# Kernel optimization log

Measured on AMD Instinct MI355X. Metric: run time of the kernel, lower is better.

The kernel has to match this reference:

```python
import jax, jax.numpy as jnp
import numpy as np

B, S, D, H = 2, 2048, 1024, 16
DEPTH = D // H


def setup_inputs() -> dict:
    key = jax.random.key(0)
    ks = jax.random.split(key, 6)
    q = jax.random.normal(ks[0], (B, S, D), dtype=jnp.float32)
    k = jax.random.normal(ks[1], (B, S, D), dtype=jnp.float32)
    v = jax.random.normal(ks[2], (B, S, D), dtype=jnp.float32)
    # causal mask, broadcastable to [B, H, S, S]
    mask = jnp.tril(jnp.ones((S, S), dtype=bool))[None, None, :, :]
    wq = jax.random.normal(ks[3], (D, D), dtype=jnp.float32)
    wk = jax.random.normal(ks[4], (D, D), dtype=jnp.float32)
    wv = jax.random.normal(ks[5], (D, D), dtype=jnp.float32)
    return {"q": q, "k": k, "v": v, "mask": mask, "wq": wq, "wk": wk, "wv": wv}


def _split_heads(x):
    # [B, S, D] -> [B, H, S, depth]
    return x.reshape(x.shape[0], -1, H, DEPTH).transpose(0, 2, 1, 3)


def reference(q, k, v, mask, wq, wk, wv):
    q = _split_heads(q @ wq)
    k = _split_heads(k @ wk)
    v = _split_heads(v @ wv)
    scale = jnp.sqrt(jnp.float32(DEPTH))
    # [B, H, S, S]
    scores = jnp.einsum("bhqd,bhkd->bhqk", q, k) / scale
    scores = jnp.where(mask, scores, jnp.float32(-8.0))
    scores = scores - jnp.max(scores, axis=-1, keepdims=True)
    attn = jax.nn.softmax(scores, axis=-1)
    out = jnp.einsum("bhqk,bhkd->bhqd", attn, v)
    # [B, H, S, depth] -> [B, S, D]
    return out.transpose(0, 2, 1, 3).reshape(out.shape[0], -1, D)
```

## Files before the change

kernel.cpp:

```cpp
#include <hip/hip_runtime.h>
#include <hip/hip_bf16.h>

#define B_  2
#define S_  2048
#define D_  1024
#define H_  16
#define DH_ 64

typedef __attribute__((ext_vector_type(8)))  short  short8;
typedef __attribute__((ext_vector_type(4)))  short  short4b;
typedef __attribute__((ext_vector_type(16))) float  f32x16;

#define MFMA32(A,B,C) __builtin_amdgcn_mfma_f32_32x32x16_bf16(A,B,C,0,0,0)

static __device__ __forceinline__ short bf16b(float x) {
    __hip_bfloat16 h = __float2bfloat16(x);
    return *(short*)&h;
}
static __device__ __forceinline__ float bf16tof(short s) {
    union { unsigned u; float f; } cv;
    cv.u = ((unsigned)(unsigned short)s) << 16;
    return cv.f;
}
static __device__ __forceinline__ void gl2lds(const short* g, short* l) {
    __builtin_amdgcn_global_load_lds(
        (const __attribute__((address_space(1))) unsigned int*)g,
        (__attribute__((address_space(3))) unsigned int*)l, 16, 0, 0);
}
static __device__ __forceinline__ unsigned cvtpk(float a, float b) {
    unsigned r;
    asm("v_cvt_pk_bf16_f32 %0, %1, %2" : "=v"(r) : "v"(a), "v"(b));
    return r;
}
static __device__ __forceinline__ void pl32swap(unsigned &a, unsigned &b) {
    asm volatile("v_permlane32_swap_b32 %0, %1" : "+v"(a), "+v"(b));
}

__global__ __launch_bounds__(256)
void conv_all(const float* __restrict__ q, const float* __restrict__ k,
              const float* __restrict__ v,
              const float* __restrict__ wq, const float* __restrict__ wk,
              const float* __restrict__ wv, char* __restrict__ ws) {
    __shared__ short HiT[64][80];
    __shared__ short LoT[64][80];
    const int bid = blockIdx.x;
    const int t   = threadIdx.x;
    if (bid < 12288) {
        const int z   = bid >> 12;
        const int xb  = bid & 4095;
        const float* src = z == 0 ? q : z == 1 ? k : v;
        short* hi = (short*)(ws + (size_t)z * 16777216);
        short* lo = hi + 4194304;
        const int i = (xb * 256 + t) * 4;
        float4 xv = *(const float4*)&src[i];
        const float* xf = (const float*)&xv;
        short4b h4, l4;
#pragma unroll
        for (int e = 0; e < 4; ++e) {
            short hb = bf16b(xf[e]);
            h4[e] = hb;
            l4[e] = bf16b(xf[e] - bf16tof(hb));
        }
        *(short4b*)&hi[i] = h4;
        *(short4b*)&lo[i] = l4;
        return;
    }
    const int wid = bid - 12288;
    const int z   = wid >> 8;
    const int rem = wid & 255;
    const int k0  = (rem & 15) << 6, n0 = (rem >> 4) << 6;
    const float* w = z == 0 ? wq : z == 1 ? wk : wv;
    short* oh = (short*)(ws + 50331648 + (size_t)z * 4194304);
    short* ol = oh + 1048576;

    const int kr = t >> 2, c4 = (t & 3) * 16;
    const float* srow = w + (size_t)(k0 + kr) * 1024 + n0 + c4;
#pragma unroll
    for (int u = 0; u < 16; u += 4) {
        float4 f = *(const float4*)&srow[u];
        const float* ff = (const float*)&f;
#pragma unroll
        for (int e = 0; e < 4; ++e) {
            int nl = c4 + u + e;
            short hb = bf16b(ff[e]);
            HiT[nl][kr] = hb;
            LoT[nl][kr] = bf16b(ff[e] - bf16tof(hb));
        }
    }
    __syncthreads();
    const int nl = t >> 2, kc = (t & 3) * 16;
    size_t off = (size_t)(n0 + nl) * 1024 + k0 + kc;
    *(short8*)&oh[off]     = *(const short8*)&HiT[nl][kc];
    *(short8*)&oh[off + 8] = *(const short8*)&HiT[nl][kc + 8];
    *(short8*)&ol[off]     = *(const short8*)&LoT[nl][kc];
    *(short8*)&ol[off + 8] = *(const short8*)&LoT[nl][kc + 8];
}

#define AH_ 0
#define AL_ 8192
#define BH_ 16384
#define BL_ 24576

__global__ __launch_bounds__(512, 2)
void proj_mfma(const short* __restrict__ xh0, const short* __restrict__ xl0,
               const short* __restrict__ xh1, const short* __restrict__ xl1,
               const short* __restrict__ xh2, const short* __restrict__ xl2,
               const short* __restrict__ wh0, const short* __restrict__ wl0,
               const short* __restrict__ wh1, const short* __restrict__ wl1,
               const short* __restrict__ wh2, const short* __restrict__ wl2,
               short* __restrict__ qh, short* __restrict__ ql,
               short* __restrict__ kh, short* __restrict__ kl,
               short* __restrict__ vt) {
    __shared__ __align__(16) short lds[65536];
    const int z  = blockIdx.z;
    const int m0 = blockIdx.y * 256;
    const int n0 = blockIdx.x * 256;
    const int t = threadIdx.x, lane = t & 63, w = t >> 6;
    const int l31 = lane & 31, hh = lane >> 5;
    const int wr = w >> 2, wc = w & 3;

    const short* xh = z == 0 ? xh0 : z == 1 ? xh1 : xh2;
    const short* xl = z == 0 ? xl0 : z == 1 ? xl1 : xl2;
    const short* wh = z == 0 ? wh0 : z == 1 ? wh1 : wh2;
    const short* wl = z == 0 ? wl0 : z == 1 ? wl1 : wl2;

    const short* gs[8];
    short*       ld8[8];
#pragma unroll
    for (int j = 0; j < 8; ++j) {
        const int arr = j >> 1;
        const int cc  = t + ((j & 1) << 9);
        const int row = cc >> 2, p = cc & 3;
        const int kc  = p ^ ((row & 3) ^ ((row >> 2) & 3));
        const short* base = arr == 0 ? xh : arr == 1 ? xl : arr == 2 ? wh : wl;
        const int r0g = (arr < 2) ? m0 : n0;
        gs[j]  = base + (size_t)(r0g + row) * 1024 + kc * 8;
        ld8[j] = &lds[arr * 8192 + ((j & 1) << 12) + (w << 9)];
    }

    const int swl = (l31 & 3) ^ ((l31 >> 2) & 3);
    const int co0 = (hh ^ swl) << 3;
    const int co1 = ((2 | hh) ^ swl) << 3;
    int rA[4], rB[2];
#pragma unroll
    for (int p = 0; p < 4; ++p) rA[p] = (wr * 128 + p * 32 + l31) * 32;
#pragma unroll
    for (int n = 0; n < 2; ++n) rB[n] = (wc * 64 + n * 32 + l31) * 32;

    f32x16 acc[4][2] = {};

#pragma unroll
    for (int j = 0; j < 8; ++j)
        gl2lds(gs[j], ld8[j]);
    asm volatile("s_waitcnt vmcnt(0)" ::: "memory");
    __builtin_amdgcn_s_barrier();

#define PHASE_MFMA(PA, PB)                                                    \
    acc[PA][0] = MFMA32(ah0, bh0k, acc[PA][0]);                               \
    acc[PA][1] = MFMA32(ah0, bh1k, acc[PA][1]);                               \
    acc[PB][0] = MFMA32(ah1, bh0k, acc[PB][0]);                               \
    acc[PB][1] = MFMA32(ah1, bh1k, acc[PB][1]);                               \
    acc[PA][0] = MFMA32(ah0, bl0k, acc[PA][0]);                               \
    acc[PA][1] = MFMA32(ah0, bl1k, acc[PA][1]);                               \
    acc[PB][0] = MFMA32(ah1, bl0k, acc[PB][0]);                               \
    acc[PB][1] = MFMA32(ah1, bl1k, acc[PB][1]);                               \
    acc[PA][0] = MFMA32(al0, bh0k, acc[PA][0]);                               \
    acc[PA][1] = MFMA32(al0, bh1k, acc[PA][1]);                               \
    acc[PB][0] = MFMA32(al1, bh0k, acc[PB][0]);                               \
    acc[PB][1] = MFMA32(al1, bh1k, acc[PB][1]);

    for (int kt = 0; kt < 32; ++kt) {
        const int tb = (kt & 1) << 15;
        const int nbo = 32768 - tb;
        const int nk = (kt + 1) * 32;
        const bool st = (kt < 31);

        short8 bh0k, bh1k, bl0k, bl1k, ah0, ah1, al0, al1;

        __builtin_amdgcn_sched_barrier(0);
        bh0k = *(const short8*)&lds[tb + BH_ + rB[0] + co0];
        bh1k = *(const short8*)&lds[tb + BH_ + rB[1] + co0];
        bl0k = *(const short8*)&lds[tb + BL_ + rB[0] + co0];
        bl1k = *(const short8*)&lds[tb + BL_ + rB[1] + co0];
        ah0  = *(const short8*)&lds[tb + AH_ + rA[0] + co0];
        ah1  = *(const short8*)&lds[tb + AH_ + rA[1] + co0];
        al0  = *(const short8*)&lds[tb + AL_ + rA[0] + co0];
        al1  = *(const short8*)&lds[tb + AL_ + rA[1] + co0];
        if (st) { gl2lds(gs[0] + nk, ld8[0] + nbo);
                  gl2lds(gs[1] + nk, ld8[1] + nbo); }
        __builtin_amdgcn_s_barrier();
        asm volatile("s_waitcnt lgkmcnt(0)" ::: "memory");
        __builtin_amdgcn_sched_barrier(0);
        __builtin_amdgcn_s_setprio(1);
        PHASE_MFMA(0, 1)
        __builtin_amdgcn_s_setprio(0);
        __builtin_amdgcn_sched_barrier(0);
        __builtin_amdgcn_s_barrier();

        __builtin_amdgcn_sched_barrier(0);
        ah0 = *(const short8*)&lds[tb + AH_ + rA[2] + co0];
        ah1 = *(const short8*)&lds[tb + AH_ + rA[3] + co0];
        al0 = *(const short8*)&lds[tb + AL_ + rA[2] + co0];
        al1 = *(const short8*)&lds[tb + AL_ + rA[3] + co0];
        if (st) { gl2lds(gs[2] + nk, ld8[2] + nbo);
                  gl2lds(gs[3] + nk, ld8[3] + nbo); }
        __builtin_amdgcn_s_barrier();
        asm volatile("s_waitcnt lgkmcnt(0)" ::: "memory");
        __builtin_amdgcn_sched_barrier(0);
        __builtin_amdgcn_s_setprio(1);
        PHASE_MFMA(2, 3)
        __builtin_amdgcn_s_setprio(0);
        __builtin_amdgcn_sched_barrier(0);
        __builtin_amdgcn_s_barrier();

        __builtin_amdgcn_sched_barrier(0);
        bh0k = *(const short8*)&lds[tb + BH_ + rB[0] + co1];
        bh1k = *(const short8*)&lds[tb + BH_ + rB[1] + co1];
        bl0k = *(const short8*)&lds[tb + BL_ + rB[0] + co1];
        bl1k = *(const short8*)&lds[tb + BL_ + rB[1] + co1];
        ah0  = *(const short8*)&lds[tb + AH_ + rA[0] + co1];
        ah1  = *(const short8*)&lds[tb + AH_ + rA[1] + co1];
        al0  = *(const short8*)&lds[tb + AL_ + rA[0] + co1];
        al1  = *(const short8*)&lds[tb + AL_ + rA[1] + co1];
        if (st) { gl2lds(gs[4] + nk, ld8[4] + nbo);
                  gl2lds(gs[5] + nk, ld8[5] + nbo);
                  gl2lds(gs[6] + nk, ld8[6] + nbo);
                  gl2lds(gs[7] + nk, ld8[7] + nbo); }
        __builtin_amdgcn_s_barrier();
        asm volatile("s_waitcnt lgkmcnt(0)" ::: "memory");
        __builtin_amdgcn_sched_barrier(0);
        __builtin_amdgcn_s_setprio(1);
        PHASE_MFMA(0, 1)
        __builtin_amdgcn_s_setprio(0);
        __builtin_amdgcn_sched_barrier(0);
        __builtin_amdgcn_s_barrier();

        __builtin_amdgcn_sched_barrier(0);
        ah0 = *(const short8*)&lds[tb + AH_ + rA[2] + co1];
        ah1 = *(const short8*)&lds[tb + AH_ + rA[3] + co1];
        al0 = *(const short8*)&lds[tb + AL_ + rA[2] + co1];
        al1 = *(const short8*)&lds[tb + AL_ + rA[3] + co1];
        __builtin_amdgcn_s_barrier();
        asm volatile("s_waitcnt lgkmcnt(0)" ::: "memory");
        __builtin_amdgcn_sched_barrier(0);
        __builtin_amdgcn_s_setprio(1);
        PHASE_MFMA(2, 3)
        __builtin_amdgcn_s_setprio(0);
        __builtin_amdgcn_sched_barrier(0);
        asm volatile("s_waitcnt vmcnt(0)" ::: "memory");
        __builtin_amdgcn_s_barrier();
    }
#undef PHASE_MFMA

    const int bb = m0 >> 11;
    const int sbase = (m0 & 2047) + wr * 128;
    if (z < 2) {
        short* oh = z == 0 ? qh : kh;
        short* ol = z == 0 ? ql : kl;
        const float qs = (z == 0) ? 0.125f : 1.0f;
#pragma unroll
        for (int p = 0; p < 4; ++p)
#pragma unroll
        for (int nt = 0; nt < 2; ++nt) {
            int n_g = n0 + wc * 64 + nt * 32 + l31;
            int h = n_g >> 6, d = n_g & 63;
#pragma unroll
            for (int r = 0; r < 16; ++r) {
                int s = sbase + p * 32 + (r & 3) + 8 * (r >> 2) + 4 * hh;
                size_t off = (((size_t)(bb * 16 + h) * 2048 + s) << 6) + d;
                float a = acc[p][nt][r] * qs;
                short hb = bf16b(a);
                oh[off] = hb;
                ol[off] = bf16b(a - bf16tof(hb));
            }
        }
    } else {
#pragma unroll
        for (int p = 0; p < 4; ++p)
#pragma unroll
        for (int nt = 0; nt < 2; ++nt) {
            int n_g = n0 + wc * 64 + nt * 32 + l31;
            int h = n_g >> 6, d = n_g & 63;
            size_t vbase = ((size_t)(bb * 16 + h) * 64 + d) * 2048;
#pragma unroll
            for (int r2 = 0; r2 < 4; ++r2) {
                int s0 = sbase + p * 32 + 8 * r2 + 4 * hh;
                short4b pk;
#pragma unroll
                for (int a2 = 0; a2 < 4; ++a2)
                    pk[a2] = bf16b(acc[p][nt][r2 * 4 + a2]);
                *(short4b*)&vt[vbase + s0] = pk;
            }
        }
    }
}

__global__ __launch_bounds__(256, 2)
void attn_mfma(const short* __restrict__ Qhi, const short* __restrict__ Qlo,
               const short* __restrict__ Khi, const short* __restrict__ Klo,
               const short* __restrict__ Vt,  float* __restrict__ out) {
    __shared__ __align__(16) short SBUF[24576];
    __shared__ float svp[4][64];
    __shared__ float svs[64];
#define KhiS (SBUF)
#define KloS (SBUF + 8192)
#define VtS  (SBUF + 16384)

    const int t     = threadIdx.x;
    const int lane  = t & 63;
    const int w     = t >> 6;
    const int l31   = lane & 31;
    const int hh    = lane >> 5;
    const int bh    = blockIdx.x;
    const int yy    = blockIdx.y;
    const int qt    = (yy < 8) ? yy : 23 - yy;
    const int q0    = qt * 128;
    const int myq   = q0 + w * 32 + l31;
    const int myq_min = q0 + w * 32;
    const int ktend = 2 * qt + 2;

    const size_t basebh = (size_t)bh * S_ * DH_;

    {
        const int s_begin = ktend * 64;
        float part = 0.f;
        const short* vrow = Vt + basebh + (size_t)lane * S_;
        for (int s = s_begin + w * 8; s < S_; s += 32) {
            short8 vv = *(const short8*)&vrow[s];
#pragma unroll
            for (int e = 0; e < 8; ++e) part += bf16tof(vv[e]);
        }
        svp[w][lane] = part;
    }
    __syncthreads();
    if (t < 64)
        svs[t] = svp[0][t] + svp[1][t] + svp[2][t] + svp[3][t];

    short8 qh[4], ql[4];
    {
        const short* qr = Qhi + basebh + (size_t)myq * DH_;
        const short* lr = Qlo + basebh + (size_t)myq * DH_;
#pragma unroll
        for (int kf = 0; kf < 4; ++kf) {
            int dofs = kf * 16 + hh * 8;
            qh[kf] = *(const short8*)(qr + dofs);
            ql[kf] = *(const short8*)(lr + dofs);
        }
    }

    const int i1 = (w << 6) | lane;
    const int i2 = 256 + i1;
    const int r1 = i1 >> 3, c1 = (i1 & 7) ^ (r1 & 7);
    const int r2 = i2 >> 3, c2 = (i2 & 7) ^ (r2 & 7);
    const short* gKh1 = Khi + basebh + (size_t)r1 * 64 + c1 * 8;
    const short* gKh2 = Khi + basebh + (size_t)r2 * 64 + c2 * 8;
    const short* gKl1 = Klo + basebh + (size_t)r1 * 64 + c1 * 8;
    const short* gKl2 = Klo + basebh + (size_t)r2 * 64 + c2 * 8;
    const short* gV1  = Vt  + basebh + (size_t)r1 * S_ + c1 * 8;
    const short* gV2  = Vt  + basebh + (size_t)r2 * S_ + c2 * 8;
    const int wub = w << 9;

#define ASTAGE(KT, BUF) do {                                                  \
        const int ka_ = (KT) * 4096, va_ = (KT) * 64, bo_ = (BUF) * 4096;     \
        gl2lds(gKh1 + ka_, &KhiS[bo_ + wub]);                                 \
        gl2lds(gKh2 + ka_, &KhiS[bo_ + 2048 + wub]);                          \
        gl2lds(gKl1 + ka_, &KloS[bo_ + wub]);                                 \
        gl2lds(gKl2 + ka_, &KloS[bo_ + 2048 + wub]);                          \
        gl2lds(gV1  + va_, &VtS [bo_ + wub]);                                 \
        gl2lds(gV2  + va_, &VtS [bo_ + 2048 + wub]);                          \
    } while (0)

    float m_run = -INFINITY, l_run = 0.f;
    f32x16 oT0 = {}, oT1 = {};

    const int sw0 = l31 & 7;

    ASTAGE(0, 0);

    for (int kt = 0; kt < ktend; ++kt) {
        const int bo = (kt & 1) << 12;
        asm volatile("s_waitcnt vmcnt(0)" ::: "memory");
        __builtin_amdgcn_s_barrier();
        __builtin_amdgcn_sched_barrier(0);
        if (kt + 1 < ktend)
            ASTAGE(kt + 1, (kt & 1) ^ 1);
        __builtin_amdgcn_sched_barrier(0);

        f32x16 acc0 = {}, acc1 = {};
        __builtin_amdgcn_s_setprio(1);
#pragma unroll
        for (int kf = 0; kf < 4; ++kf) {
            const int cs = ((2 * kf + hh) ^ sw0) << 3;
            short8 k0h = *(const short8*)&KhiS[bo + l31 * 64 + cs];
            short8 k0l = *(const short8*)&KloS[bo + l31 * 64 + cs];
            short8 k1h = *(const short8*)&KhiS[bo + (l31 + 32) * 64 + cs];
            short8 k1l = *(const short8*)&KloS[bo + (l31 + 32) * 64 + cs];
            acc0 = MFMA32(k0h, qh[kf], acc0);
            acc0 = MFMA32(k0h, ql[kf], acc0);
            acc0 = MFMA32(k0l, qh[kf], acc0);
            acc1 = MFMA32(k1h, qh[kf], acc1);
            acc1 = MFMA32(k1h, ql[kf], acc1);
            acc1 = MFMA32(k1l, qh[kf], acc1);
        }
        __builtin_amdgcn_s_setprio(0);

        float vals[32];
        float tmax;
        if (kt * 64 + 63 <= myq_min) {
            float t0 = -INFINITY, t1 = -INFINITY;
#pragma unroll
            for (int r = 0; r < 16; ++r) {
                vals[r]      = acc0[r];
                vals[16 + r] = acc1[r];
                t0 = fmaxf(t0, acc0[r]);
                t1 = fmaxf(t1, acc1[r]);
            }
            tmax = fmaxf(t0, t1);
        } else {
            tmax = -INFINITY;
#pragma unroll
            for (int r = 0; r < 16; ++r) {
                int key0 = kt * 64 + ((r & 3) + 8 * (r >> 2) + 4 * hh);
                float v0 = (key0 <= myq)      ? acc0[r] : -8.0f;
                float v1 = (key0 + 32 <= myq) ? acc1[r] : -8.0f;
                vals[r] = v0;
                vals[16 + r] = v1;
                tmax = fmaxf(tmax, fmaxf(v0, v1));
            }
        }
        tmax = fmaxf(tmax, __shfl_xor(tmax, 32, 64));
        const bool defer = __all(tmax <= m_run + 8.0f);
        if (!defer) {
            float mnew  = fmaxf(m_run, tmax);
            float alpha = __expf(m_run - mnew);
            l_run *= alpha;
#pragma unroll
            for (int r = 0; r < 16; ++r) { oT0[r] *= alpha; oT1[r] *= alpha; }
            m_run = mnew;
        }
        float psum = 0.f;
        unsigned cw[16];
#pragma unroll
        for (int tt = 0; tt < 16; ++tt) {
            float p0 = __expf(vals[2 * tt]     - m_run);
            float p1 = __expf(vals[2 * tt + 1] - m_run);
            psum += p0 + p1;
            cw[tt] = cvtpk(p0, p1);
        }
        psum += __shfl_xor(psum, 32, 64);
        l_run += psum;

        __builtin_amdgcn_s_setprio(1);
#pragma unroll
        for (int kf = 0; kf < 4; ++kf) {
            unsigned w0 = cw[4 * kf],     w1 = cw[4 * kf + 1];
            unsigned w2 = cw[4 * kf + 2], w3 = cw[4 * kf + 3];
            pl32swap(w0, w2);
            pl32swap(w1, w3);
            union { unsigned u[4]; short8 s8; } pu;
            pu.u[0] = w0; pu.u[1] = w1; pu.u[2] = w2; pu.u[3] = w3;
            const int cs = ((2 * kf + hh) ^ sw0) << 3;
            short8 v0 = *(const short8*)&VtS[bo + l31 * 64 + cs];
            short8 v1 = *(const short8*)&VtS[bo + (l31 + 32) * 64 + cs];
            oT0 = MFMA32(v0, pu.s8, oT0);
            oT1 = MFMA32(v1, pu.s8, oT1);
        }
        __builtin_amdgcn_s_setprio(0);
        __builtin_amdgcn_sched_barrier(0);
    }
#undef ASTAGE

    {
        float mfin = fmaxf(m_run, -8.0f);
        float aa   = __expf(m_run - mfin);
        float e8   = __expf(-8.0f - mfin);
        float nrem = (float)(S_ - ktend * 64);
        float lfin = l_run * aa + nrem * e8;
        float inv  = 1.0f / lfin;
#pragma unroll
        for (int r = 0; r < 16; ++r) {
            int dim0 = (r & 3) + 8 * (r >> 2) + 4 * hh;
            oT0[r] = (oT0[r] * aa + e8 * svs[dim0])      * inv;
            oT1[r] = (oT1[r] * aa + e8 * svs[dim0 + 32]) * inv;
        }
    }

    __syncthreads();
    float* Ob = (float*)SBUF + w * 2176;
#pragma unroll
    for (int r = 0; r < 16; ++r) {
        int dim0 = (r & 3) + 8 * (r >> 2) + 4 * hh;
        Ob[l31 * 68 + dim0]      = oT0[r];
        Ob[l31 * 68 + dim0 + 32] = oT1[r];
    }
    {
        const int qq = lane >> 1;
        const int ch = (lane & 1) * 32;
        const float* src = Ob + qq * 68 + ch;
        const int b  = bh >> 4;
        const int h  = bh & 15;
        float* dst = out + ((size_t)b * S_ + (q0 + w * 32 + qq)) * D_ + h * 64 + ch;
#pragma unroll
        for (int c = 0; c < 32; c += 4)
            *(float4*)(dst + c) = *(const float4*)(src + c);
    }
#undef KhiS
#undef KloS
#undef VtS
}

extern "C" void kernel_launch(void* const* d_in, const int* in_sizes, int n_in,
                              void* d_out, int out_size, void* d_ws, size_t ws_size,
                              hipStream_t stream) {
    const float* q  = (const float*)d_in[0];
    const float* k  = (const float*)d_in[1];
    const float* v  = (const float*)d_in[2];
    const float* wq = (const float*)d_in[4];
    const float* wk = (const float*)d_in[5];
    const float* wv = (const float*)d_in[6];
    float* out = (float*)d_out;

    char* ws = (char*)d_ws;
    const short* XH[3] = {(short*)ws, (short*)(ws + 16777216), (short*)(ws + 33554432)};
    const short* XL[3] = {XH[0] + 4194304, XH[1] + 4194304, XH[2] + 4194304};
    const short* WH[3] = {(short*)(ws + 50331648), (short*)(ws + 54525952), (short*)(ws + 58720256)};
    const short* WL[3] = {WH[0] + 1048576, WH[1] + 1048576, WH[2] + 1048576};

    short *Qhi, *Qlo, *Khi, *Klo, *Vt;
    if (ws_size >= (size_t)104857600) {
        Qhi = (short*)(ws + 62914560);
        Qlo = (short*)(ws + 71303168);
        Khi = (short*)(ws + 79691776);
        Klo = (short*)(ws + 88080384);
        Vt  = (short*)(ws + 96468992);
    } else {
        Qhi = (short*)d_in[0]; Qlo = Qhi + 4194304;
        Khi = (short*)d_in[1]; Klo = Khi + 4194304;
        Vt  = (short*)d_in[2];
    }

    conv_all<<<dim3(13056), 256, 0, stream>>>(q, k, v, wq, wk, wv, ws);

    proj_mfma<<<dim3(4, 16, 3), 512, 0, stream>>>(
        XH[0], XL[0], XH[1], XL[1], XH[2], XL[2],
        WH[0], WL[0], WH[1], WL[1], WH[2], WL[2],
        Qhi, Qlo, Khi, Klo, Vt);

    attn_mfma<<<dim3(32, 16), 256, 0, stream>>>(Qhi, Qlo, Khi, Klo, Vt, out);
}
```

Baseline: 266.4 us.

## Split long causal query tiles across two blocks with a combine kernel

New measurement: 275.3 us. 1.03x slower.

```diff
diff --git a/kernel.cpp b/kernel.cpp
--- a/kernel.cpp
+++ b/kernel.cpp
@@ -298,7 +298,8 @@
 __global__ __launch_bounds__(256, 2)
 void attn_mfma(const short* __restrict__ Qhi, const short* __restrict__ Qlo,
                const short* __restrict__ Khi, const short* __restrict__ Klo,
-               const short* __restrict__ Vt,  float* __restrict__ out) {
+               const short* __restrict__ Vt,  float* __restrict__ PB,
+               float* __restrict__ out) {
     __shared__ __align__(16) short SBUF[24576];
     __shared__ float svp[4][64];
     __shared__ float svs[64];
@@ -313,7 +314,14 @@
     const int hh    = lane >> 5;
     const int bh    = blockIdx.x;
     const int yy    = blockIdx.y;
-    const int qt    = (yy < 8) ? yy : 23 - yy;
+
+    int qt, kt0, ktn;
+    bool full;
+    if (yy < 8) { qt = yy;             full = true;  kt0 = 0; ktn = 2 * qt + 2; }
+    else { int j = (yy - 8) >> 1, s = (yy - 8) & 1;
+           qt = 8 + j;                 full = false;
+           int hseg = qt + 1;          kt0 = s * hseg; ktn = hseg; }
+
     const int q0    = qt * 128;
     const int myq   = q0 + w * 32 + l31;
     const int myq_min = q0 + w * 32;
@@ -321,7 +329,7 @@
 
     const size_t basebh = (size_t)bh * S_ * DH_;
 
-    {
+    if (full) {
         const int s_begin = ktend * 64;
         float part = 0.f;
         const short* vrow = Vt + basebh + (size_t)lane * S_;
@@ -331,10 +339,10 @@
             for (int e = 0; e < 8; ++e) part += bf16tof(vv[e]);
         }
         svp[w][lane] = part;
-    }
-    __syncthreads();
-    if (t < 64)
-        svs[t] = svp[0][t] + svp[1][t] + svp[2][t] + svp[3][t];
+        __syncthreads();
+        if (t < 64)
+            svs[t] = svp[0][t] + svp[1][t] + svp[2][t] + svp[3][t];
+    }
 
     short8 qh[4], ql[4];
     {
@@ -375,15 +383,16 @@
 
     const int sw0 = l31 & 7;
 
-    ASTAGE(0, 0);
-
-    for (int kt = 0; kt < ktend; ++kt) {
-        const int bo = (kt & 1) << 12;
+    ASTAGE(kt0, 0);
+
+    for (int idx = 0; idx < ktn; ++idx) {
+        const int kt = kt0 + idx;
+        const int bo = (idx & 1) << 12;
         asm volatile("s_waitcnt vmcnt(0)" ::: "memory");
         __builtin_amdgcn_s_barrier();
         __builtin_amdgcn_sched_barrier(0);
-        if (kt + 1 < ktend)
-            ASTAGE(kt + 1, (kt & 1) ^ 1);
+        if (idx + 1 < ktn)
+            ASTAGE(kt + 1, (idx & 1) ^ 1);
         __builtin_amdgcn_sched_barrier(0);
 
         f32x16 acc0 = {}, acc1 = {};
@@ -470,6 +479,20 @@
     }
 #undef ASTAGE
 
+    if (!full) {
+        const int j = qt - 8, s = (kt0 != 0);
+        float* seg = PB + (((size_t)bh * 8 + j) * 2 + s) * 8448;
+        const int row = w * 32 + l31;
+#pragma unroll
+        for (int r = 0; r < 16; ++r) {
+            int d0 = (r & 3) + 8 * (r >> 2) + 4 * hh;
+            seg[row * 64 + d0]      = oT0[r];
+            seg[row * 64 + d0 + 32] = oT1[r];
+        }
+        if (hh == 0) { seg[8192 + row] = m_run; seg[8320 + row] = l_run; }
+        return;
+    }
+
     {
         float mfin = fmaxf(m_run, -8.0f);
         float aa   = __expf(m_run - mfin);
@@ -507,6 +530,61 @@
 #undef KhiS
 #undef KloS
 #undef VtS
+}
+
+__global__ __launch_bounds__(256)
+void attn_combine(const float* __restrict__ PB, const short* __restrict__ Vt,
+                  float* __restrict__ out) {
+    __shared__ float svp[4][64];
+    __shared__ float svs[64];
+    const int bh = blockIdx.x >> 3, j = blockIdx.x & 7;
+    const int qt = 8 + j, ktend = 2 * qt + 2;
+    const int nrem = S_ - ktend * 64;
+    const int t = threadIdx.x;
+
+    {
+        const int d = t & 63, g = t >> 6;
+        float part = 0.f;
+        const short* vrow = Vt + (size_t)bh * DH_ * S_ + (size_t)d * S_;
+        for (int s = ktend * 64 + g * 8; s < S_; s += 32) {
+            short8 vv = *(const short8*)&vrow[s];
+#pragma unroll
+            for (int e = 0; e < 8; ++e) part += bf16tof(vv[e]);
+        }
+        svp[g][d] = part;
+    }
+    __syncthreads();
+    if (t < 64) svs[t] = svp[0][t] + svp[1][t] + svp[2][t] + svp[3][t];
+    __syncthreads();
+
+    const float* s0 = PB + (((size_t)bh * 8 + j) * 2) * 8448;
+    const float* s1 = s0 + 8448;
+    const int row = t >> 1, half = (t & 1) * 32;
+
+    const float m0 = s0[8192 + row], l0 = s0[8320 + row];
+    const float m1 = s1[8192 + row], l1 = s1[8320 + row];
+    const float m    = fmaxf(m0, m1);
+    const float mfin = fmaxf(m, -8.0f);
+    const float a0 = __expf(m0 - mfin), a1 = __expf(m1 - mfin);
+    const float e8 = __expf(-8.0f - mfin);
+    const float lfin = l0 * a0 + l1 * a1 + (float)nrem * e8;
+    const float inv = 1.0f / lfin;
+
+    const int b = bh >> 4, h = bh & 15;
+    float* dst = out + ((size_t)b * S_ + qt * 128 + row) * D_ + h * 64 + half;
+    const float* O0 = s0 + row * 64 + half;
+    const float* O1 = s1 + row * 64 + half;
+#pragma unroll
+    for (int c = 0; c < 32; c += 4) {
+        float4 o0 = *(const float4*)(O0 + c);
+        float4 o1 = *(const float4*)(O1 + c);
+        float4 r;
+        r.x = (o0.x * a0 + o1.x * a1 + e8 * svs[half + c + 0]) * inv;
+        r.y = (o0.y * a0 + o1.y * a1 + e8 * svs[half + c + 1]) * inv;
+        r.z = (o0.z * a0 + o1.z * a1 + e8 * svs[half + c + 2]) * inv;
+        r.w = (o0.w * a0 + o1.w * a1 + e8 * svs[half + c + 3]) * inv;
+        *(float4*)(dst + c) = r;
+    }
 }
 
 extern "C" void kernel_launch(void* const* d_in, const int* in_sizes, int n_in,
@@ -525,6 +603,8 @@
     const short* XL[3] = {XH[0] + 4194304, XH[1] + 4194304, XH[2] + 4194304};
     const short* WH[3] = {(short*)(ws + 50331648), (short*)(ws + 54525952), (short*)(ws + 58720256)};
     const short* WL[3] = {WH[0] + 1048576, WH[1] + 1048576, WH[2] + 1048576};
+
+    float* PB = (float*)ws;
 
     short *Qhi, *Qlo, *Khi, *Klo, *Vt;
     if (ws_size >= (size_t)104857600) {
@@ -546,5 +626,7 @@
         WH[0], WL[0], WH[1], WL[1], WH[2], WL[2],
         Qhi, Qlo, Khi, Klo, Vt);
 
-    attn_mfma<<<dim3(32, 16), 256, 0, stream>>>(Qhi, Qlo, Khi, Klo, Vt, out);
-}
+    attn_mfma<<<dim3(32, 24), 256, 0, stream>>>(Qhi, Qlo, Khi, Klo, Vt, PB, out);
+
+    attn_combine<<<dim3(256), 256, 0, stream>>>(PB, Vt, out);
+}
```
